# Optimization experiments

Measured on AMD Instinct MI355X. Metric: run time of the kernel, lower is better.

The kernel has to match this reference:

```python
import jax, jax.numpy as jnp
import numpy as np

B, T, D_ENC, D_FEAT, D_WORD, H, V = 512, 80, 1024, 512, 512, 512, 10000


def setup_inputs() -> dict:
    key = jax.random.key(0)
    ks = jax.random.split(key, 8)
    s = 0.02
    return {
        "outputs_encoder": jax.random.normal(ks[0], (B, T, D_ENC), jnp.float32),
        "start_ids": jax.random.randint(ks[1], (B,), 0, V, jnp.int32),
        "W_proj": jax.random.normal(ks[2], (D_ENC, D_FEAT), jnp.float32) * s,
        "b_proj": jnp.zeros((D_FEAT,), jnp.float32),
        "embed_table": jax.random.normal(ks[3], (V, D_WORD), jnp.float32) * s,
        "W_ih": jax.random.normal(ks[4], (4 * H, D_FEAT + D_WORD), jnp.float32) * s,
        "W_hh": jax.random.normal(ks[5], (4 * H, H), jnp.float32) * s,
        "b_ih": jnp.zeros((4 * H,), jnp.float32),
        "b_hh": jnp.zeros((4 * H,), jnp.float32),
    }


def _lstm_cell(x, h, c, W_ih, W_hh, b_ih, b_hh):
    # torch.nn.LSTMCell gate order: i, f, g, o
    gates = x @ W_ih.T + b_ih + h @ W_hh.T + b_hh  # [B, 4H]
    i, f, g, o = jnp.split(gates, 4, axis=-1)
    c_new = jax.nn.sigmoid(f) * c + jax.nn.sigmoid(i) * jnp.tanh(g)
    h_new = jax.nn.sigmoid(o) * jnp.tanh(c_new)
    return h_new, c_new


def reference(outputs_encoder, start_ids, W_proj, b_proj, embed_table, W_ih, W_hh, b_ih, b_hh):
    # project encoder features: [B, T, D_FEAT]
    feats = jnp.einsum("btd,df->btf", outputs_encoder, W_proj) + b_proj
    word = embed_table[start_ids]  # [B, D_WORD] (<start> embedding, reused each step)
    h0 = jnp.zeros((feats.shape[0], W_hh.shape[1]), feats.dtype)
    c0 = jnp.zeros_like(h0)

    def step(carry, feat_t):
        h, c = carry
        x = jnp.concatenate([feat_t, word], axis=1)  # [B, D_FEAT+D_WORD]
        h, c = _lstm_cell(x, h, c, W_ih, W_hh, b_ih, b_hh)
        return (h, c), h

    (_, _), hs = jax.lax.scan(step, (h0, c0), jnp.swapaxes(feats, 0, 1))  # hs: [T, B, H]
    return jnp.swapaxes(hs, 0, 1)  # [B, T, H]
```

## Files before the change

kernel.cpp:

```cpp
#include <hip/hip_runtime.h>
#include <stdint.h>

typedef __bf16 bf16x8 __attribute__((ext_vector_type(8)));
typedef float  f32x4  __attribute__((ext_vector_type(4)));
typedef unsigned int u32x4 __attribute__((ext_vector_type(4)));
typedef unsigned long long u64;

__device__ __forceinline__ uint16_t f2b(float f) {
  uint32_t u = __float_as_uint(f);
  return (uint16_t)((u + 0x7FFFu + ((u >> 16) & 1u)) >> 16);
}
__device__ __forceinline__ float b2f(uint16_t h) {
  return __uint_as_float(((uint32_t)h) << 16);
}
__device__ __forceinline__ uint4 pack8f(float4 a, float4 b) {
  uint4 r;
  r.x = (uint32_t)f2b(a.x) | ((uint32_t)f2b(a.y) << 16);
  r.y = (uint32_t)f2b(a.z) | ((uint32_t)f2b(a.w) << 16);
  r.z = (uint32_t)f2b(b.x) | ((uint32_t)f2b(b.y) << 16);
  r.w = (uint32_t)f2b(b.z) | ((uint32_t)f2b(b.w) << 16);
  return r;
}
__device__ __forceinline__ float fsig(float x) {
  return 1.f / (1.f + __expf(-x));
}
__device__ __forceinline__ float ftanh(float x) {
  return 1.f - 2.f / (1.f + __expf(2.f * x));
}
__device__ __forceinline__ void gload_lds16(const void* g, void* l) {
  __builtin_amdgcn_global_load_lds(
      (const __attribute__((address_space(1))) uint32_t*)g,
      (__attribute__((address_space(3))) uint32_t*)l, 16, 0, 0);
}

__global__ void detect_kernel(const uint32_t* __restrict__ wproj, int* flag) {
  __shared__ int cnt;
  if (threadIdx.x == 0) cnt = 0;
  __syncthreads();
  int local = 0;
  for (int i = threadIdx.x; i < 1024; i += 256) {
    float v = __uint_as_float((wproj[i] & 0xFFFFu) << 16);
    float av = fabsf(v);
    if (av > 1e-4f && av < 0.5f) local++;
  }
  atomicAdd(&cnt, local);
  __syncthreads();
  if (threadIdx.x == 0) flag[0] = (cnt > 512) ? 1 : 0;
}

__global__ void convert_kernel(const void* __restrict__ src,
                               uint16_t* __restrict__ dst,
                               const int* __restrict__ flagp) {
  int i = blockIdx.x * 256 + threadIdx.x;
  if (*flagp) {
    ((uint4*)dst)[i] = ((const uint4*)src)[i];
  } else {
    const float* s = (const float*)src + (size_t)i * 8;
    ((uint4*)dst)[i] = pack8f(*(const float4*)s, *(const float4*)(s + 4));
  }
}

__global__ void convA_kernel(const void* __restrict__ enc,
                             uint16_t* __restrict__ encb,
                             const int* __restrict__ flagp, int c0) {
  int i = blockIdx.x * 256 + threadIdx.x;
  int m = i >> 7, ch = i & 127;
  int b = m >> 4, t0 = m & 15;
  size_t src = ((size_t)b * 80 + c0 + t0) * 1024 + (size_t)ch * 8;
  if (*flagp) {
    ((uint4*)encb)[i] = *(const uint4*)((const uint16_t*)enc + src);
  } else {
    const float* s = (const float*)enc + src;
    ((uint4*)encb)[i] = pack8f(*(const float4*)s, *(const float4*)(s + 4));
  }
}

__global__ void word_kernel(const int* __restrict__ ids,
                            const void* __restrict__ embed,
                            uint16_t* __restrict__ word,
                            const int* __restrict__ flagp) {
  int c = blockIdx.x * 256 + threadIdx.x;
  int b = c >> 6, off = c & 63;
  size_t row = (size_t)ids[b] * 512;
  if (*flagp) {
    ((uint4*)word)[c] = ((const uint4*)((const uint16_t*)embed + row))[off];
  } else {
    const float* s = (const float*)embed + row + (size_t)off * 8;
    ((uint4*)word)[c] = pack8f(*(const float4*)s, *(const float4*)(s + 4));
  }
}

__global__ void bias2_kernel(const void* __restrict__ bih,
                             const void* __restrict__ bhh,
                             const void* __restrict__ bproj,
                             const uint16_t* __restrict__ Wihb,
                             float* __restrict__ bias2,
                             const int* __restrict__ flagp) {
  const int wid = threadIdx.x >> 6, lane = threadIdx.x & 63;
  const int j = blockIdx.x * 4 + wid;
  const int fl = *flagp;
  uint4 wv = *(const uint4*)(Wihb + (size_t)j * 1024 + lane * 8);
  const uint16_t wh[8] = {
      (uint16_t)wv.x, (uint16_t)(wv.x >> 16), (uint16_t)wv.y, (uint16_t)(wv.y >> 16),
      (uint16_t)wv.z, (uint16_t)(wv.z >> 16), (uint16_t)wv.w, (uint16_t)(wv.w >> 16)};
  float bp[8];
  if (fl) {
    uint4 pv = *(const uint4*)((const uint16_t*)bproj + lane * 8);
    const uint16_t ph[8] = {
        (uint16_t)pv.x, (uint16_t)(pv.x >> 16), (uint16_t)pv.y, (uint16_t)(pv.y >> 16),
        (uint16_t)pv.z, (uint16_t)(pv.z >> 16), (uint16_t)pv.w, (uint16_t)(pv.w >> 16)};
#pragma unroll
    for (int e = 0; e < 8; e++) bp[e] = b2f(ph[e]);
  } else {
    float4 p0 = ((const float4*)bproj)[lane * 2];
    float4 p1 = ((const float4*)bproj)[lane * 2 + 1];
    bp[0] = p0.x; bp[1] = p0.y; bp[2] = p0.z; bp[3] = p0.w;
    bp[4] = p1.x; bp[5] = p1.y; bp[6] = p1.z; bp[7] = p1.w;
  }
  float acc = 0.f;
#pragma unroll
  for (int e = 0; e < 8; e++) acc += bp[e] * b2f(wh[e]);
#pragma unroll
  for (int m = 32; m >= 1; m >>= 1) acc += __shfl_xor(acc, m, 64);
  if (lane == 0) {
    float s;
    if (fl) s = b2f(((const uint16_t*)bih)[j]) + b2f(((const uint16_t*)bhh)[j]);
    else    s = ((const float*)bih)[j] + ((const float*)bhh)[j];
    bias2[j] = s + acc;
  }
}

template <int MODE>
__global__ __launch_bounds__(256, 2)
void gemm_bt(const uint16_t* __restrict__ A, int lda,
             const uint16_t* __restrict__ Bt, int ldb,
             void* __restrict__ Cout, int ldc, int K,
             const float* __restrict__ wg) {
  __shared__ __align__(16) uint16_t As[128 * 32];
  __shared__ __align__(16) uint16_t Bs[128 * 32];
  const int tid = threadIdx.x;
  const int bm = blockIdx.y * 128, bn = blockIdx.x * 128;
  const int wid = tid >> 6, lane = tid & 63;
  const int wm = (wid >> 1) * 64, wn = (wid & 1) * 64;
  const int lrow = lane & 15, quad = lane >> 4;
  const int srow = tid >> 2, scol = (tid & 3) * 8;

  const uint16_t* ga0 = A + (size_t)(bm + srow) * lda + scol;
  const uint16_t* ga1 = A + (size_t)(bm + 64 + srow) * lda + scol;
  const uint16_t* gb0 = Bt + (size_t)(bn + srow) * ldb + scol;
  const uint16_t* gb1 = Bt + (size_t)(bn + 64 + srow) * ldb + scol;
  uint16_t* la0 = As + srow * 32 + scol;
  uint16_t* la1 = As + (64 + srow) * 32 + scol;
  uint16_t* lb0 = Bs + srow * 32 + scol;
  uint16_t* lb1 = Bs + (64 + srow) * 32 + scol;

  f32x4 acc[4][4] = {};

  for (int kb = 0; kb < K; kb += 32) {
    __syncthreads();
    gload_lds16(ga0 + kb, la0);
    gload_lds16(ga1 + kb, la1);
    gload_lds16(gb0 + kb, lb0);
    gload_lds16(gb1 + kb, lb1);
    __syncthreads();
    bf16x8 af[4], bfr[4];
#pragma unroll
    for (int i = 0; i < 4; i++) {
      af[i]  = *reinterpret_cast<const bf16x8*>(As + (wm + i * 16 + lrow) * 32 + quad * 8);
      bfr[i] = *reinterpret_cast<const bf16x8*>(Bs + (wn + i * 16 + lrow) * 32 + quad * 8);
    }
#pragma unroll
    for (int i = 0; i < 4; i++)
#pragma unroll
      for (int j = 0; j < 4; j++)
        acc[i][j] = __builtin_amdgcn_mfma_f32_16x16x32_bf16(af[i], bfr[j], acc[i][j], 0, 0, 0);
  }

  if constexpr (MODE == 0) {
    uint16_t* C = (uint16_t*)Cout;
#pragma unroll
    for (int i = 0; i < 4; i++) {
      int row = bm + wm + i * 16 + quad * 4;
#pragma unroll
      for (int j = 0; j < 4; j++) {
        int col = bn + wn + j * 16 + lrow;
#pragma unroll
        for (int r = 0; r < 4; r++)
          C[(size_t)(row + r) * ldc + col] = f2b(acc[i][j][r]);
      }
    }
  } else if constexpr (MODE == 2) {
    float* C = (float*)Cout;
#pragma unroll
    for (int i = 0; i < 4; i++) {
      int row = bm + wm + i * 16 + quad * 4;
#pragma unroll
      for (int j = 0; j < 4; j++) {
        int col = bn + wn + j * 16 + lrow;
        float bias = wg[col];
#pragma unroll
        for (int r = 0; r < 4; r++)
          C[(size_t)(row + r) * ldc + col] = acc[i][j][r] + bias;
      }
    }
  } else {
    float* C = (float*)Cout;
#pragma unroll
    for (int i = 0; i < 4; i++) {
#pragma unroll
      for (int r = 0; r < 4; r++) {
        int m = bm + wm + i * 16 + quad * 4 + r;
        int b = m >> 4, t0 = m & 15;
        size_t orow = (size_t)t0 * 512 + b;
#pragma unroll
        for (int j = 0; j < 4; j++) {
          int col = bn + wn + j * 16 + lrow;
          C[orow * 2048 + col] = acc[i][j][r] + wg[(size_t)b * 2048 + col];
        }
      }
    }
  }
}

__global__ __launch_bounds__(256, 1)
void lstm16_kernel(const uint16_t* __restrict__ Whhb,
                   const float* __restrict__ xg,
                   uint16_t* __restrict__ hring,
                   float* __restrict__ cst,
                   void* __restrict__ out,
                   int tbase,
                   const int* __restrict__ flagp,
                   unsigned int* __restrict__ bar) {
  __shared__ __align__(16) uint16_t Hs[32 * 512];
  __shared__ float Gs[4][32][33];

  const int tid = threadIdx.x;
  const int bid = blockIdx.x;
  const int rb = ((bid & 7) << 1) | ((bid >> 3) & 1);
  const int cb = bid >> 4;
  const int g = tid >> 6;
  const int lane = tid & 63;
  const int lrow = lane & 15, quad = lane >> 4;
  const int fl = *flagp;

  u32x4 breg[2][16];
  {
    const uint16_t* wb = Whhb + ((size_t)(g * 512 + cb * 32 + lrow) * 512) + quad * 8;
#pragma unroll
    for (int j = 0; j < 2; j++)
#pragma unroll
      for (int kk = 0; kk < 16; kk++) {
        breg[j][kk] = *reinterpret_cast<const u32x4*>(wb + (size_t)j * 16 * 512 + kk * 32);
        asm volatile("" : "+v"(breg[j][kk]));
      }
  }

  const int erow = tid >> 3;
  const int ecol = (tid & 7) * 4;
  const int gb = rb * 32 + erow;
  const int gh = cb * 32 + ecol;
  f32x4 creg = *reinterpret_cast<const f32x4*>(cst + (size_t)gb * 512 + gh);

  const int sc16 = (tid & 7) * 16;
  const int ssw = (erow & 7) << 4;
  unsigned int* cnt = bar + rb * 64;

#pragma unroll 1
  for (int s = 0; s < 16; s++) {
    const int t = tbase + s;
    const uint16_t* hin = hring + (size_t)((t + 16) % 17) * 262144;
    uint16_t* hout = hring + (size_t)(t % 17) * 262144;

    const float* xr = xg + ((size_t)s * 512 + gb) * 2048 + gh;
    f32x4 x0 = *reinterpret_cast<const f32x4*>(xr);
    f32x4 x1 = *reinterpret_cast<const f32x4*>(xr + 512);
    f32x4 x2 = *reinterpret_cast<const f32x4*>(xr + 1024);
    f32x4 x3 = *reinterpret_cast<const f32x4*>(xr + 1536);

    {
      const char* hsrc = (const char*)(hin + (size_t)gb * 512);
      char* hdst = (char*)Hs + erow * 1024;
#pragma unroll
      for (int it = 0; it < 8; it++) {
        int bc = sc16 + it * 128;
        *reinterpret_cast<uint4*>(hdst + (bc ^ ssw)) =
            *reinterpret_cast<const uint4*>(hsrc + bc);
      }
    }
    __syncthreads();

    f32x4 acc[2][2] = {};
#pragma unroll
    for (int kk = 0; kk < 16; kk++) {
      bf16x8 af[2];
#pragma unroll
      for (int i = 0; i < 2; i++) {
        int r = i * 16 + lrow;
        int bc = kk * 64 + quad * 16;
        af[i] = *reinterpret_cast<const bf16x8*>(
            (const char*)Hs + r * 1024 + (bc ^ ((r & 7) << 4)));
      }
#pragma unroll
      for (int i = 0; i < 2; i++)
#pragma unroll
        for (int j = 0; j < 2; j++)
          acc[i][j] = __builtin_amdgcn_mfma_f32_16x16x32_bf16(
              af[i], __builtin_bit_cast(bf16x8, breg[j][kk]), acc[i][j], 0, 0, 0);
    }

#pragma unroll
    for (int i = 0; i < 2; i++)
#pragma unroll
      for (int j = 0; j < 2; j++)
#pragma unroll
        for (int r = 0; r < 4; r++)
          Gs[g][i * 16 + quad * 4 + r][j * 16 + lrow] = acc[i][j][r];
    __syncthreads();

    float hnv[4];
#pragma unroll
    for (int e = 0; e < 4; e++) {
      float p_i = Gs[0][erow][ecol + e] + x0[e];
      float p_f = Gs[1][erow][ecol + e] + x1[e];
      float p_g = Gs[2][erow][ecol + e] + x2[e];
      float p_o = Gs[3][erow][ecol + e] + x3[e];
      float si = fsig(p_i);
      float sf = fsig(p_f);
      float so = fsig(p_o);
      float tg = ftanh(p_g);
      float cn = sf * creg[e] + si * tg;
      creg[e] = cn;
      hnv[e] = so * ftanh(cn);
    }
    uint2 hp;
    hp.x = (uint32_t)f2b(hnv[0]) | ((uint32_t)f2b(hnv[1]) << 16);
    hp.y = (uint32_t)f2b(hnv[2]) | ((uint32_t)f2b(hnv[3]) << 16);
    u64 hv = (u64)hp.x | ((u64)hp.y << 32);
    __hip_atomic_store((u64*)(hout + (size_t)gb * 512 + gh), hv,
                       __ATOMIC_RELAXED, __HIP_MEMORY_SCOPE_AGENT);
    size_t oi = (size_t)gb * (80 * 512) + (size_t)t * 512 + gh;
    if (fl) {
      *reinterpret_cast<uint2*>((uint16_t*)out + oi) = hp;
    } else {
      float4 ov = make_float4(hnv[0], hnv[1], hnv[2], hnv[3]);
      *reinterpret_cast<float4*>((float*)out + oi) = ov;
    }

    __syncthreads();
    if (tid == 0) {
      __hip_atomic_fetch_add(cnt, 1u, __ATOMIC_RELAXED, __HIP_MEMORY_SCOPE_AGENT);
      if (s != 15) {
        unsigned tgt = (unsigned)(t + 1) * 16u;
        while (__hip_atomic_load(cnt, __ATOMIC_RELAXED, __HIP_MEMORY_SCOPE_AGENT) < tgt)
          __builtin_amdgcn_s_sleep(1);
      }
    }
    __syncthreads();
  }

  *reinterpret_cast<f32x4*>(cst + (size_t)gb * 512 + gh) = creg;
}

extern "C" void kernel_launch(void* const* d_in, const int* in_sizes, int n_in,
                              void* d_out, int out_size, void* d_ws, size_t ws_size,
                              hipStream_t stream) {
  const void* enc   = d_in[0];
  const int*  ids   = (const int*)d_in[1];
  const void* Wproj = d_in[2];
  const void* bproj = d_in[3];
  const void* embed = d_in[4];
  const void* Wih   = d_in[5];
  const void* Whh   = d_in[6];
  const void* bih   = d_in[7];
  const void* bhh   = d_in[8];

  uint8_t* w = (uint8_t*)d_ws;
  int*      flag   = (int*)w;
  unsigned int* bar = (unsigned int*)(w + 8192);
  float*    bias2  = (float*)(w + 16384);
  float*    wgates = (float*)(w + 32768);
  uint16_t* combT  = (uint16_t*)(w + 4227072);
  uint16_t* Wihb   = (uint16_t*)(w + 8421376);
  uint16_t* Whhb   = (uint16_t*)(w + 12615680);
  uint16_t* Wprojb = (uint16_t*)(w + 14712832);
  uint16_t* word   = (uint16_t*)(w + 15761408);
  float*    cst    = (float*)(w + 17334272);
  float*    xgbuf  = (float*)(w + 18382848);
  uint16_t* hring  = (uint16_t*)(w + 85491712);
  uint16_t* encb   = (uint16_t*)(w + 94404608);

  detect_kernel<<<1, 256, 0, stream>>>((const uint32_t*)Wproj, flag);
  convert_kernel<<<1024, 256, 0, stream>>>(Wih, Wihb, flag);
  convert_kernel<<<512, 256, 0, stream>>>(Whh, Whhb, flag);
  convert_kernel<<<256, 256, 0, stream>>>(Wproj, Wprojb, flag);
  word_kernel<<<128, 256, 0, stream>>>(ids, embed, word, flag);
  bias2_kernel<<<512, 256, 0, stream>>>(bih, bhh, bproj, Wihb, bias2, flag);

  gemm_bt<0><<<dim3(8, 16), 256, 0, stream>>>(Wihb, 1024, Wprojb, 512,
                                              combT, 1024, 512, nullptr);
  gemm_bt<2><<<dim3(16, 4), 256, 0, stream>>>(word, 512, Wihb + 512, 1024,
                                              wgates, 2048, 512, bias2);

  (void)hipMemsetAsync(hring + (size_t)16 * 262144, 0, 524288, stream);
  (void)hipMemsetAsync(cst, 0, 512 * 512 * 4, stream);
  (void)hipMemsetAsync(bar, 0, 4096, stream);

  const uint16_t* Whhb_a = Whhb;
  const float* xg_a = xgbuf;
  uint16_t* hring_a = hring;
  float* cst_a = cst;
  void* out_a = d_out;
  const int* flag_a = flag;
  unsigned int* bar_a = bar;

  for (int c = 0; c < 5; c++) {
    convA_kernel<<<4096, 256, 0, stream>>>(enc, encb, flag, c * 16);
    gemm_bt<1><<<dim3(16, 64), 256, 0, stream>>>(encb, 1024, combT, 1024,
                                                 xgbuf, 2048, 1024, wgates);
    int tbase = c * 16;
    void* kargs[] = {(void*)&Whhb_a, (void*)&xg_a, (void*)&hring_a,
                     (void*)&cst_a, (void*)&out_a, (void*)&tbase, (void*)&flag_a,
                     (void*)&bar_a};
    (void)hipLaunchCooperativeKernel(lstm16_kernel, dim3(256), dim3(256), kargs,
                                     0u, stream);
  }
}
```

Measured before the change: 958.6 us.

## Fuse input-gate GEMM into LSTM chunk kernel with producer warps

The per-chunk input-gate GEMM is removed as a separate launch and moved into extra producer waves inside the cooperative LSTM kernel. These waves compute each timestep's gate preactivations and signal completion through per-timestep counters, while the recurrent waves spin-wait on the counter before consuming that step. This is meant to overlap the large input projection with the serial recurrence and to save a launch per chunk. In exchange, the block grows to 512 threads, __syncthreads is replaced by a custom LDS barrier over only the four consumer waves, and xg is read and written with system-scope atomics, which adds ordering and occupancy risk.

```diff
diff --git a/kernel.cpp b/kernel.cpp
--- a/kernel.cpp
+++ b/kernel.cpp
@@ -64,8 +64,8 @@
                              uint16_t* __restrict__ encb,
                              const int* __restrict__ flagp, int c0) {
   int i = blockIdx.x * 256 + threadIdx.x;
-  int m = i >> 7, ch = i & 127;
-  int b = m >> 4, t0 = m & 15;
+  int mp = i >> 7, ch = i & 127;
+  int t0 = mp >> 9, b = mp & 511;
   size_t src = ((size_t)b * 80 + c0 + t0) * 1024 + (size_t)ch * 8;
   if (*flagp) {
     ((uint4*)encb)[i] = *(const uint4*)((const uint16_t*)enc + src);
@@ -189,7 +189,7 @@
           C[(size_t)(row + r) * ldc + col] = f2b(acc[i][j][r]);
       }
     }
-  } else if constexpr (MODE == 2) {
+  } else {
     float* C = (float*)Cout;
 #pragma unroll
     for (int i = 0; i < 4; i++) {
@@ -203,45 +203,87 @@
           C[(size_t)(row + r) * ldc + col] = acc[i][j][r] + bias;
       }
     }
-  } else {
-    float* C = (float*)Cout;
-#pragma unroll
-    for (int i = 0; i < 4; i++) {
-#pragma unroll
-      for (int r = 0; r < 4; r++) {
-        int m = bm + wm + i * 16 + quad * 4 + r;
-        int b = m >> 4, t0 = m & 15;
-        size_t orow = (size_t)t0 * 512 + b;
-#pragma unroll
-        for (int j = 0; j < 4; j++) {
-          int col = bn + wn + j * 16 + lrow;
-          C[orow * 2048 + col] = acc[i][j][r] + wg[(size_t)b * 2048 + col];
-        }
-      }
-    }
-  }
-}
-
-__global__ __launch_bounds__(256, 1)
-void lstm16_kernel(const uint16_t* __restrict__ Whhb,
-                   const float* __restrict__ xg,
-                   uint16_t* __restrict__ hring,
-                   float* __restrict__ cst,
-                   void* __restrict__ out,
-                   int tbase,
-                   const int* __restrict__ flagp,
-                   unsigned int* __restrict__ bar) {
+  }
+}
+
+__global__ __launch_bounds__(512, 2)
+void chunk_kernel(const uint16_t* __restrict__ Whhb,
+                  const uint16_t* __restrict__ encb,
+                  const uint16_t* __restrict__ combT,
+                  const float* __restrict__ wgates,
+                  float* __restrict__ xg,
+                  uint16_t* __restrict__ hring,
+                  float* __restrict__ cst,
+                  void* __restrict__ out,
+                  int c,
+                  const int* __restrict__ flagp,
+                  unsigned int* __restrict__ bar) {
   __shared__ __align__(16) uint16_t Hs[32 * 512];
   __shared__ float Gs[4][32][33];
-
+  __shared__ unsigned int cbar;
   const int tid = threadIdx.x;
   const int bid = blockIdx.x;
+  const int wid = tid >> 6;
+  const int lane = tid & 63;
+  const int tbase = c * 16;
+  unsigned int* done = bar + 1024;
+
+  if (tid == 0) cbar = 0u;
+  __syncthreads();
+
+  if (wid >= 4) {
+    const int pw = bid * 4 + (wid - 4);
+    const int lrow = lane & 15, quad = lane >> 4;
+#pragma unroll 1
+    for (int r = 0; r < 4; r++) {
+      const int t0 = r * 4 + (pw >> 8);
+      const int q = pw & 255;
+      const int b0 = (q & 7) * 64, j0 = (q >> 3) * 64;
+      const uint16_t* Abase = encb + ((size_t)t0 * 512 + b0 + lrow) * 1024 + quad * 8;
+      const uint16_t* Bbase = combT + ((size_t)(j0 + lrow)) * 1024 + quad * 8;
+      f32x4 acc[4][4] = {};
+      for (int kb = 0; kb < 1024; kb += 32) {
+        bf16x8 af[4], bfr[4];
+#pragma unroll
+        for (int i = 0; i < 4; i++)
+          af[i] = *reinterpret_cast<const bf16x8*>(Abase + (size_t)i * 16 * 1024 + kb);
+#pragma unroll
+        for (int j = 0; j < 4; j++)
+          bfr[j] = *reinterpret_cast<const bf16x8*>(Bbase + (size_t)j * 16 * 1024 + kb);
+#pragma unroll
+        for (int i = 0; i < 4; i++)
+#pragma unroll
+          for (int j = 0; j < 4; j++)
+            acc[i][j] = __builtin_amdgcn_mfma_f32_16x16x32_bf16(af[i], bfr[j], acc[i][j], 0, 0, 0);
+      }
+#pragma unroll
+      for (int i = 0; i < 4; i++)
+#pragma unroll
+        for (int rr = 0; rr < 4; rr++) {
+          int b = b0 + i * 16 + quad * 4 + rr;
+          float* crow = xg + ((size_t)t0 * 512 + b) * 2048;
+          const float* wrow = wgates + (size_t)b * 2048;
+#pragma unroll
+          for (int j = 0; j < 4; j++) {
+            int col = j0 + j * 16 + lrow;
+            __hip_atomic_store(crow + col, acc[i][j][rr] + wrow[col],
+                               __ATOMIC_RELAXED, __HIP_MEMORY_SCOPE_SYSTEM);
+          }
+        }
+      asm volatile("s_waitcnt vmcnt(0)" ::: "memory");
+      if (lane == 0)
+        __hip_atomic_fetch_add(&done[tbase + t0], 1u, __ATOMIC_RELAXED,
+                               __HIP_MEMORY_SCOPE_SYSTEM);
+    }
+    return;
+  }
+
   const int rb = ((bid & 7) << 1) | ((bid >> 3) & 1);
   const int cb = bid >> 4;
   const int g = tid >> 6;
-  const int lane = tid & 63;
   const int lrow = lane & 15, quad = lane >> 4;
   const int fl = *flagp;
+  unsigned int btgt = 0;
 
   u32x4 breg[2][16];
   {
@@ -265,17 +307,41 @@
   const int ssw = (erow & 7) << 4;
   unsigned int* cnt = bar + rb * 64;
 
+#define CONS_BAR()                                                            \
+  do {                                                                        \
+    btgt += 4;                                                                \
+    asm volatile("s_waitcnt vmcnt(0) lgkmcnt(0)" ::: "memory");               \
+    if (lane == 0)                                                            \
+      __hip_atomic_fetch_add(&cbar, 1u, __ATOMIC_RELEASE,                     \
+                             __HIP_MEMORY_SCOPE_WORKGROUP);                   \
+    while (__hip_atomic_load(&cbar, __ATOMIC_ACQUIRE,                         \
+                             __HIP_MEMORY_SCOPE_WORKGROUP) < btgt)            \
+      __builtin_amdgcn_s_sleep(1);                                            \
+  } while (0)
+
 #pragma unroll 1
   for (int s = 0; s < 16; s++) {
     const int t = tbase + s;
     const uint16_t* hin = hring + (size_t)((t + 16) % 17) * 262144;
     uint16_t* hout = hring + (size_t)(t % 17) * 262144;
 
-    const float* xr = xg + ((size_t)s * 512 + gb) * 2048 + gh;
-    f32x4 x0 = *reinterpret_cast<const f32x4*>(xr);
-    f32x4 x1 = *reinterpret_cast<const f32x4*>(xr + 512);
-    f32x4 x2 = *reinterpret_cast<const f32x4*>(xr + 1024);
-    f32x4 x3 = *reinterpret_cast<const f32x4*>(xr + 1536);
+    if (s == 0) {
+      if (tid == 0)
+        while (__hip_atomic_load(&done[t], __ATOMIC_RELAXED,
+                                 __HIP_MEMORY_SCOPE_SYSTEM) < 256u)
+          __builtin_amdgcn_s_sleep(1);
+      CONS_BAR();
+    }
+
+    const u64* xq = (const u64*)(xg + ((size_t)s * 512 + gb) * 2048 + gh);
+    u64 q0 = __hip_atomic_load(xq + 0,   __ATOMIC_RELAXED, __HIP_MEMORY_SCOPE_SYSTEM);
+    u64 q1 = __hip_atomic_load(xq + 1,   __ATOMIC_RELAXED, __HIP_MEMORY_SCOPE_SYSTEM);
+    u64 q2 = __hip_atomic_load(xq + 256, __ATOMIC_RELAXED, __HIP_MEMORY_SCOPE_SYSTEM);
+    u64 q3 = __hip_atomic_load(xq + 257, __ATOMIC_RELAXED, __HIP_MEMORY_SCOPE_SYSTEM);
+    u64 q4 = __hip_atomic_load(xq + 512, __ATOMIC_RELAXED, __HIP_MEMORY_SCOPE_SYSTEM);
+    u64 q5 = __hip_atomic_load(xq + 513, __ATOMIC_RELAXED, __HIP_MEMORY_SCOPE_SYSTEM);
+    u64 q6 = __hip_atomic_load(xq + 768, __ATOMIC_RELAXED, __HIP_MEMORY_SCOPE_SYSTEM);
+    u64 q7 = __hip_atomic_load(xq + 769, __ATOMIC_RELAXED, __HIP_MEMORY_SCOPE_SYSTEM);
 
     {
       const char* hsrc = (const char*)(hin + (size_t)gb * 512);
@@ -287,7 +353,7 @@
             *reinterpret_cast<const uint4*>(hsrc + bc);
       }
     }
-    __syncthreads();
+    CONS_BAR();
 
     f32x4 acc[2][2] = {};
 #pragma unroll
@@ -315,8 +381,17 @@
 #pragma unroll
         for (int r = 0; r < 4; r++)
           Gs[g][i * 16 + quad * 4 + r][j * 16 + lrow] = acc[i][j][r];
-    __syncthreads();
-
+    CONS_BAR();
+
+    f32x4 x0, x1, x2, x3;
+    { float2 a = __builtin_bit_cast(float2, q0), b = __builtin_bit_cast(float2, q1);
+      x0[0] = a.x; x0[1] = a.y; x0[2] = b.x; x0[3] = b.y; }
+    { float2 a = __builtin_bit_cast(float2, q2), b = __builtin_bit_cast(float2, q3);
+      x1[0] = a.x; x1[1] = a.y; x1[2] = b.x; x1[3] = b.y; }
+    { float2 a = __builtin_bit_cast(float2, q4), b = __builtin_bit_cast(float2, q5);
+      x2[0] = a.x; x2[1] = a.y; x2[2] = b.x; x2[3] = b.y; }
+    { float2 a = __builtin_bit_cast(float2, q6), b = __builtin_bit_cast(float2, q7);
+      x3[0] = a.x; x3[1] = a.y; x3[2] = b.x; x3[3] = b.y; }
     float hnv[4];
 #pragma unroll
     for (int e = 0; e < 4; e++) {
@@ -346,17 +421,20 @@
       *reinterpret_cast<float4*>((float*)out + oi) = ov;
     }
 
-    __syncthreads();
+    CONS_BAR();
     if (tid == 0) {
       __hip_atomic_fetch_add(cnt, 1u, __ATOMIC_RELAXED, __HIP_MEMORY_SCOPE_AGENT);
       if (s != 15) {
         unsigned tgt = (unsigned)(t + 1) * 16u;
-        while (__hip_atomic_load(cnt, __ATOMIC_RELAXED, __HIP_MEMORY_SCOPE_AGENT) < tgt)
+        while (__hip_atomic_load(cnt, __ATOMIC_RELAXED, __HIP_MEMORY_SCOPE_AGENT) < tgt ||
+               __hip_atomic_load(&done[t + 1], __ATOMIC_RELAXED,
+                                 __HIP_MEMORY_SCOPE_SYSTEM) < 256u)
           __builtin_amdgcn_s_sleep(1);
       }
     }
-    __syncthreads();
-  }
+    CONS_BAR();
+  }
+#undef CONS_BAR
 
   *reinterpret_cast<f32x4*>(cst + (size_t)gb * 512 + gh) = creg;
 }
@@ -403,10 +481,13 @@
 
   (void)hipMemsetAsync(hring + (size_t)16 * 262144, 0, 524288, stream);
   (void)hipMemsetAsync(cst, 0, 512 * 512 * 4, stream);
-  (void)hipMemsetAsync(bar, 0, 4096, stream);
+  (void)hipMemsetAsync(bar, 0, 8192, stream);
 
   const uint16_t* Whhb_a = Whhb;
-  const float* xg_a = xgbuf;
+  const uint16_t* encb_a = encb;
+  const uint16_t* combT_a = combT;
+  const float* wgates_a = wgates;
+  float* xg_a = xgbuf;
   uint16_t* hring_a = hring;
   float* cst_a = cst;
   void* out_a = d_out;
@@ -415,13 +496,12 @@
 
   for (int c = 0; c < 5; c++) {
     convA_kernel<<<4096, 256, 0, stream>>>(enc, encb, flag, c * 16);
-    gemm_bt<1><<<dim3(16, 64), 256, 0, stream>>>(encb, 1024, combT, 1024,
-                                                 xgbuf, 2048, 1024, wgates);
-    int tbase = c * 16;
-    void* kargs[] = {(void*)&Whhb_a, (void*)&xg_a, (void*)&hring_a,
-                     (void*)&cst_a, (void*)&out_a, (void*)&tbase, (void*)&flag_a,
-                     (void*)&bar_a};
-    (void)hipLaunchCooperativeKernel(lstm16_kernel, dim3(256), dim3(256), kargs,
+    int cc = c;
+    void* kargs[] = {(void*)&Whhb_a, (void*)&encb_a, (void*)&combT_a,
+                     (void*)&wgates_a, (void*)&xg_a, (void*)&hring_a,
+                     (void*)&cst_a, (void*)&out_a, (void*)&cc,
+                     (void*)&flag_a, (void*)&bar_a};
+    (void)hipLaunchCooperativeKernel(chunk_kernel, dim3(256), dim3(512), kargs,
                                      0u, stream);
   }
 }
```

Result: slower. 2.566 ms (+167.7%).
